# Performance work log

Hardware: AMD Instinct MI355X
Metric: run time of the kernel (lower is better)

## Reference

```python
import jax, jax.numpy as jnp
import numpy as np

HID = 3072; HEADS = 24; HD = HID // HEADS; MLP = 4 * HID; RANK = 32
B = 1; L = 2048


def setup_inputs():
    key = jax.random.key(0)
    ks = jax.random.split(key, 16)
    def rn(i, shape, s):
        return jax.random.normal(ks[i], shape, dtype=jnp.float32) * s
    x = jax.random.normal(ks[0], (B, L, HID), dtype=jnp.float32)
    vec = jax.random.normal(ks[1], (B, HID), dtype=jnp.float32)
    # Flux-style rope rotation matrices: pe shape (1, 1, L, HD//2, 2, 2)
    pos = jnp.arange(L, dtype=jnp.float32)
    inv_freq = 1.0 / (10000.0 ** (jnp.arange(HD // 2, dtype=jnp.float32) / (HD // 2)))
    ang = pos[:, None] * inv_freq[None, :]
    cos, sin = jnp.cos(ang), jnp.sin(ang)
    pe = jnp.stack([jnp.stack([cos, -sin], -1), jnp.stack([sin, cos], -1)], -2)[None, None]
    return {
        "x": x, "vec": vec, "pe": pe,
        "mod_w": rn(2, (3 * HID, HID), 0.02), "mod_b": jnp.zeros((3 * HID,), jnp.float32),
        "w1": rn(3, (3 * HID + MLP, HID), 0.02), "b1": jnp.zeros((3 * HID + MLP,), jnp.float32),
        "w2": rn(4, (HID, HID + MLP), 0.02), "b2": jnp.zeros((HID,), jnp.float32),
        "q_scale": jnp.ones((HD,), jnp.float32), "k_scale": jnp.ones((HD,), jnp.float32),
        "lora_q_down": rn(5, (RANK, HID), 1.0 / RANK), "lora_q_up": rn(6, (HID, RANK), 0.02),
        "lora_k_down": rn(7, (RANK, HID), 1.0 / RANK), "lora_k_up": rn(8, (HID, RANK), 0.02),
        "lora_v_down": rn(9, (RANK, HID), 1.0 / RANK), "lora_v_up": rn(10, (HID, RANK), 0.02),
        "proj_down": rn(11, (2 * RANK, HID + MLP), 1.0 / (2 * RANK)),
        "proj_up": rn(12, (HID, 2 * RANK), 0.02),
    }


def _rms(t, scale, eps=1e-6):
    # QKNorm: per-head-dim RMSNorm with learnable scale
    return t * jax.lax.rsqrt(jnp.mean(t * t, axis=-1, keepdims=True) + eps) * scale


def _rope(t, pe):
    # t: (B, H, L, D); pe: (1, 1, L, D//2, 2, 2)
    tr = t.reshape(*t.shape[:-1], -1, 1, 2)
    out = pe[..., 0] * tr[..., 0] + pe[..., 1] * tr[..., 1]
    return out.reshape(t.shape)


def reference(x, vec, pe, mod_w, mod_b, w1, b1, w2, b2, q_scale, k_scale,
              lora_q_down, lora_q_up, lora_k_down, lora_k_up,
              lora_v_down, lora_v_up, proj_down, proj_up):
    lora_w = 1.0  # lora_weight; note network_alpha/rank == 1 for the defaults
    # Modulation: Linear(SiLU(vec)) -> shift, scale, gate, each (B, 1, HID)
    m = jax.nn.silu(vec) @ mod_w.T + mod_b
    shift, scale, gate = [s[:, None, :] for s in jnp.split(m, 3, axis=-1)]
    # pre_norm: LayerNorm without affine, eps=1e-6
    mu = jnp.mean(x, axis=-1, keepdims=True)
    var = jnp.mean((x - mu) ** 2, axis=-1, keepdims=True)
    x_mod = (1.0 + scale) * ((x - mu) * jax.lax.rsqrt(var + 1e-6)) + shift
    # linear1 -> qkv | mlp split
    h = x_mod @ w1.T + b1                                        # (B, L, 3*HID+MLP)
    qkv, mlp = h[..., :3 * HID], h[..., 3 * HID:]
    qkv = qkv.reshape(B, L, 3, HEADS, HD).transpose(2, 0, 3, 1, 4)  # (3, B, H, L, D)
    q, k, v = qkv[0], qkv[1], qkv[2]
    def lora(down, up):
        y = ((x_mod @ down.T) @ up.T) * lora_w                   # (B, L, HID)
        return y.reshape(B, L, HEADS, HD).transpose(0, 2, 1, 3)  # (B, H, L, D)
    q = q + lora(lora_q_down, lora_q_up)
    k = k + lora(lora_k_down, lora_k_up)
    v = v + lora(lora_v_down, lora_v_up)
    q = _rms(q, q_scale)
    k = _rms(k, k_scale)
    # Bank write (self.bank_img_{q,k,v} = q, k, v) is state capture, not math.
    q = _rope(q, pe)
    k = _rope(k, pe)
    # SDPA
    scores = jnp.einsum('bhqd,bhkd->bhqk', q, k) / jnp.sqrt(jnp.float32(HD))
    attn = jax.nn.softmax(scores, axis=-1)
    attn_out = jnp.einsum('bhqk,bhkd->bhqd', attn, v)
    attn_out = attn_out.transpose(0, 2, 1, 3).reshape(B, L, HID)  # B L (H D)
    cat = jnp.concatenate([attn_out, jax.nn.gelu(mlp, approximate=True)], axis=-1)
    out = cat @ w2.T + b2
    out = out + ((cat @ proj_down.T) @ proj_up.T) * lora_w
    return x + gate * out
```

## Files before the change

kernel.cpp:

```cpp
#include <hip/hip_runtime.h>
#include <math.h>

typedef unsigned short u16;
typedef unsigned int u32;
typedef unsigned long long u64;
typedef __attribute__((ext_vector_type(4))) float f32x4;
typedef __attribute__((ext_vector_type(8))) __bf16 bf16x8;

#define SEQ 2048
#define N1 21504
#define K1 3072
#define CATK 15360

__device__ __forceinline__ u16 f2bf(float f){
  u32 u = __float_as_uint(f);
  u32 r = u + 0x7FFFu + ((u >> 16) & 1u);
  return (u16)(r >> 16);
}
__device__ __forceinline__ float bf2f(u16 h){
  return __uint_as_float(((u32)h) << 16);
}
__device__ __forceinline__ void gl_lds16(const void* g, void* l){
  __builtin_amdgcn_global_load_lds(
      (const __attribute__((address_space(1))) void*)(size_t)g,
      (__attribute__((address_space(3))) void*)(u32)(size_t)l, 16, 0, 0);
}
__device__ __forceinline__ f32x4 zero4(){ f32x4 z; z[0]=0.f; z[1]=0.f; z[2]=0.f; z[3]=0.f; return z; }

__global__ void __launch_bounds__(256) cast_w1_tail(
    const float* __restrict__ w1, u16* __restrict__ out)
{
  int gid = blockIdx.x*256 + threadIdx.x;
  int n = 9216 + gid / 384;
  int k8 = (gid - (n-9216)*384) * 8;
  const float* src = &w1[(size_t)n*K1 + k8];
  union { u16 u[8]; uint4 q; } t;
  #pragma unroll
  for (int j=0;j<8;j++) t.u[j] = f2bf(src[j]);
  *(uint4*)&out[(size_t)n*K1 + k8] = t.q;
}

__global__ void __launch_bounds__(256) build_ustack(
    const float* __restrict__ lqu, const float* __restrict__ lku,
    const float* __restrict__ lvu, u16* __restrict__ out)
{
  int gid = blockIdx.x*256 + threadIdx.x;
  int n = gid >> 4;
  int k8 = (gid & 15) * 8;
  int b = n / 3072;
  const float* up = (b==0)? lqu : (b==1)? lku : lvu;
  int nl = n - b*3072;
  union { u16 u[8]; uint4 q; } t;
  #pragma unroll
  for (int j=0;j<8;j++){
    int r = k8 + j - 32*b;
    t.u[j] = (r >= 0 && r < 32) ? f2bf(up[(size_t)nl*32 + r]) : (u16)0;
  }
  *(uint4*)&out[(size_t)n*128 + k8] = t.q;
}

__global__ void __launch_bounds__(256) build_dcatT(
    const float* __restrict__ lqd, const float* __restrict__ lkd,
    const float* __restrict__ lvd, u16* __restrict__ out)
{
  int gid = blockIdx.x*256 + threadIdx.x;
  int k = gid >> 4;
  int r8 = (gid & 15) * 8;
  union { u16 u[8]; uint4 q; } t;
  #pragma unroll
  for (int j=0;j<8;j++){
    int r = r8 + j;
    float v = (r < 32) ? lqd[(size_t)r*3072 + k]
            : (r < 64) ? lkd[(size_t)(r-32)*3072 + k]
            : (r < 96) ? lvd[(size_t)(r-64)*3072 + k] : 0.f;
    t.u[j] = f2bf(v);
  }
  *(uint4*)&out[(size_t)k*128 + r8] = t.q;
}

__global__ void __launch_bounds__(256) build_pubf(
    const float* __restrict__ pu, u16* __restrict__ out)
{
  int gid = blockIdx.x*256 + threadIdx.x;
  int n = gid >> 3;
  int r8 = (gid & 7) * 8;
  union { u16 u[8]; uint4 q; } t;
  #pragma unroll
  for (int j=0;j<8;j++) t.u[j] = f2bf(pu[(size_t)n*64 + r8 + j]);
  *(uint4*)&out[(size_t)n*64 + r8] = t.q;
}

__global__ void __launch_bounds__(256) build_pdT(
    const float* __restrict__ pd, u16* __restrict__ out)
{
  int gid = blockIdx.x*256 + threadIdx.x;
  int jj = gid >> 3;
  int r8 = (gid & 7) * 8;
  union { u16 u[8]; uint4 q; } t;
  #pragma unroll
  for (int j=0;j<8;j++) t.u[j] = f2bf(pd[(size_t)(r8+j)*15360 + jj]);
  *(uint4*)&out[(size_t)jj*64 + r8] = t.q;
}

__global__ void __launch_bounds__(256) silu_kernel(const float* __restrict__ v, float* __restrict__ sv){
  int i = blockIdx.x*256 + threadIdx.x;
  float x = v[i];
  sv[i] = x / (1.f + __expf(-x));
}

__global__ void __launch_bounds__(256) modgemv_kernel(
    const float* __restrict__ sv, const float* __restrict__ mw,
    const float* __restrict__ mb, float* __restrict__ mout)
{
  int n = blockIdx.x, tid = threadIdx.x;
  const float* wr = mw + (size_t)n*3072;
  float p = 0.f;
  for (int c = tid; c < 3072; c += 256) p += sv[c]*wr[c];
  #pragma unroll
  for (int o=32;o>0;o>>=1) p += __shfl_down(p,o,64);
  __shared__ float red[4];
  if ((tid & 63)==0) red[tid>>6] = p;
  __syncthreads();
  if (tid==0) mout[n] = red[0]+red[1]+red[2]+red[3] + mb[n];
}

__global__ void __launch_bounds__(256) xmod_kernel(
    const float* __restrict__ x, const float* __restrict__ m, u16* __restrict__ xm)
{
  int l = blockIdx.x, tid = threadIdx.x;
  const float* xr = x + (size_t)l*3072;
  float s1=0.f, s2=0.f;
  for (int c=tid;c<3072;c+=256){ float v = xr[c]; s1+=v; s2+=v*v; }
  #pragma unroll
  for (int o=32;o>0;o>>=1){ s1 += __shfl_down(s1,o,64); s2 += __shfl_down(s2,o,64); }
  __shared__ float r1[4], r2[4];
  if ((tid&63)==0){ r1[tid>>6]=s1; r2[tid>>6]=s2; }
  __syncthreads();
  float su = r1[0]+r1[1]+r1[2]+r1[3];
  float sq = r2[0]+r2[1]+r2[2]+r2[3];
  float mu = su / 3072.f;
  float var = sq/3072.f - mu*mu;
  float rstd = rsqrtf(var + 1e-6f);
  u16* orow = xm + (size_t)l*K1;
  for (int c=tid;c<3072;c+=256){
    float v = (xr[c]-mu)*rstd;
    v = v*(1.f + m[3072+c]) + m[c];
    orow[c] = f2bf(v);
  }
}

__global__ void __launch_bounds__(256) gelu_kernel(const u16* __restrict__ h, u16* __restrict__ cat){
  int j = blockIdx.x*256 + threadIdx.x;
  int l = blockIdx.y;
  float v = bf2f(h[(size_t)l*N1 + 9216 + j]);
  float u = 0.7978845608028654f * (v + 0.044715f*v*v*v);
  float t = 1.f - 2.f/(__expf(2.f*u) + 1.f);
  cat[(size_t)l*CATK + 3072 + j] = f2bf(0.5f*v*(1.f + t));
}

__global__ void __launch_bounds__(128) qkv_kernel(
    const u16* __restrict__ h, const float* __restrict__ pe,
    const float* __restrict__ qs, const float* __restrict__ ks,
    u16* __restrict__ qbf, u16* __restrict__ kbf)
{
  const int l = blockIdx.x, hh = blockIdx.y, d = threadIdx.x;
  __shared__ float lq[128], lk[128];
  __shared__ float red[4];
  size_t base = (size_t)l*N1 + (size_t)hh*128 + d;
  float qv = bf2f(h[base]);
  float kv = bf2f(h[base + 3072]);
  float pq = qv*qv, pk = kv*kv;
  #pragma unroll
  for (int o=32;o>0;o>>=1){ pq += __shfl_down(pq,o,64); pk += __shfl_down(pk,o,64); }
  if ((d & 63)==0){ red[(d>>6)*2] = pq; red[(d>>6)*2+1] = pk; }
  __syncthreads();
  float rq = rsqrtf((red[0]+red[2])/128.f + 1e-6f);
  float rk = rsqrtf((red[1]+red[3])/128.f + 1e-6f);
  lq[d] = qv*rq*qs[d];
  lk[d] = kv*rk*ks[d];
  __syncthreads();
  int i = d >> 1;
  const float* peb = pe + ((size_t)l*64 + i)*4 + (size_t)(d&1)*2;
  float qo = peb[0]*lq[2*i] + peb[1]*lq[2*i+1];
  float ko = peb[0]*lk[2*i] + peb[1]*lk[2*i+1];
  size_t ob = ((size_t)hh*SEQ + l)*128 + d;
  qbf[ob] = f2bf(qo);
  kbf[ob] = f2bf(ko);
}

template<int MODE>
__global__ void __launch_bounds__(256) gemm_bt(
    const u16* __restrict__ A, const u16* __restrict__ B, void* __restrict__ C,
    int K, int lda, int ldb, int ldc, int ldadd,
    const float* __restrict__ bias, const float* __restrict__ xres,
    const float* __restrict__ gate)
{
  __shared__ u16 sA[128*64];
  __shared__ u16 sB[128*64];
  const int tid = threadIdx.x;
  const int lane = tid & 63;
  const int wv = tid >> 6;
  const int quad = lane >> 4;
  const int l16 = lane & 15;
  const int rw = (wv >> 1) * 64;
  const int cw = (wv & 1) * 64;
  const int m0 = blockIdx.x * 128;
  const int n0 = blockIdx.y * 128;

  f32x4 acc[4][4];
  #pragma unroll
  for (int i=0;i<4;i++){
    #pragma unroll
    for (int j=0;j<4;j++) acc[i][j] = zero4();
  }

  for (int kb = 0; kb < K; kb += 64){
    #pragma unroll
    for (int i=0;i<4;i++){
      int c = i*256 + tid, r = c >> 3, s = c & 7, g = s ^ (r & 7);
      gl_lds16(A + (size_t)(m0 + r)*lda + kb + g*8, &sA[c*8]);
    }
    #pragma unroll
    for (int i=0;i<4;i++){
      int c = i*256 + tid, r = c >> 3, s = c & 7, g = s ^ (r & 7);
      gl_lds16(B + (size_t)(n0 + r)*ldb + kb + g*8, &sB[c*8]);
    }
    __syncthreads();
    #pragma unroll
    for (int kc=0; kc<2; kc++){
      bf16x8 af[4], bfr[4];
      #pragma unroll
      for (int mt=0; mt<4; mt++){
        int row = rw + mt*16 + l16;
        int s = (kc*4 + quad) ^ (row & 7);
        af[mt] = *(const bf16x8*)&sA[row*64 + s*8];
      }
      #pragma unroll
      for (int nt=0; nt<4; nt++){
        int row = cw + nt*16 + l16;
        int s = (kc*4 + quad) ^ (row & 7);
        bfr[nt] = *(const bf16x8*)&sB[row*64 + s*8];
      }
      #pragma unroll
      for (int mt=0; mt<4; mt++){
        #pragma unroll
        for (int nt=0; nt<4; nt++)
          acc[mt][nt] = __builtin_amdgcn_mfma_f32_16x16x32_bf16(af[mt], bfr[nt], acc[mt][nt], 0, 0, 0);
      }
    }
    __syncthreads();
  }

  #pragma unroll
  for (int mt=0; mt<4; mt++){
    #pragma unroll
    for (int nt=0; nt<4; nt++){
      #pragma unroll
      for (int r=0;r<4;r++){
        int row = m0 + rw + mt*16 + quad*4 + r;
        int col = n0 + cw + nt*16 + l16;
        float v = acc[mt][nt][r];
        if (MODE==0){
          v += bias[col];
          ((u16*)C)[(size_t)row*ldc + col] = f2bf(v);
        } else if (MODE==1){
          v += bias[col];
          ((float*)C)[(size_t)row*ldc + col] = xres[(size_t)row*3072 + col] + gate[col]*v;
        } else {
          v += xres[(size_t)row*ldadd + col];
          ((u16*)C)[(size_t)row*ldc + col] = f2bf(v);
        }
      }
    }
  }
}


#define CFENCE asm volatile("" ::: "memory")
#define VMCNT(n) asm volatile("s_waitcnt vmcnt(" #n ")" ::: "memory")

__device__ __forceinline__ void stA64(const u16* __restrict__ g, u16* __restrict__ lds,
                                      int rb, int kb, int lda, int tid){
  int ri = tid >> 3, s = tid & 7;
  int R = rb + ri;
  gl_lds16(g + (size_t)R*lda + kb + ((s ^ (R & 7)) << 3), &lds[(R << 6) + (s << 3)]);
}
__device__ __forceinline__ void stB32x2(const u16* __restrict__ g, u16* __restrict__ lds,
                                        int rb, int kb, int ldb, int tid){
  int ri = tid >> 3, s = tid & 7;
  int R = rb + (ri & 31) + ((ri >> 5) << 6);
  gl_lds16(g + (size_t)R*ldb + kb + ((s ^ (R & 7)) << 3), &lds[(R << 6) + (s << 3)]);
}

__global__ void __launch_bounds__(512, 2) gemm256_bias(
    const u16* __restrict__ A, const u16* __restrict__ B, u16* __restrict__ C,
    int K, int lda, int ldb, int ldc, const float* __restrict__ bias)
{
  __shared__ u16 sA[2][256*64];
  __shared__ u16 sB[2][256*64];
  const int tid  = threadIdx.x;
  const int lane = tid & 63;
  const int wv   = tid >> 6;
  const int quad = lane >> 4;
  const int l16  = lane & 15;
  const int wm   = wv >> 2;
  const int wn   = wv & 3;
  const int m0   = blockIdx.x * 256;
  const int n0   = blockIdx.y * 256;
  const u16* Ab  = A + (size_t)m0 * lda;
  const u16* Bb  = B + (size_t)n0 * ldb;
  const int NT   = K >> 6;

  f32x4 acc[8][4];
  #pragma unroll
  for (int i=0;i<8;i++){
    #pragma unroll
    for (int j=0;j<4;j++) acc[i][j] = zero4();
  }

  stA64 (Ab, sA[0],   0, 0, lda, tid);  stA64 (Ab, sA[0], 128, 0, lda, tid);
  stB32x2(Bb, sB[0],  0, 0, ldb, tid);  stB32x2(Bb, sB[0], 128, 0, ldb, tid);
  stA64 (Ab, sA[0],  64, 0, lda, tid);  stA64 (Ab, sA[0], 192, 0, lda, tid);
  stB32x2(Bb, sB[0], 32, 0, ldb, tid);  stB32x2(Bb, sB[0], 160, 0, ldb, tid);
  if (NT > 1){
    stA64 (Ab, sA[1],   0, 64, lda, tid);  stA64 (Ab, sA[1], 128, 64, lda, tid);
    stB32x2(Bb, sB[1],  0, 64, ldb, tid);  stB32x2(Bb, sB[1], 128, 64, ldb, tid);
  }
  VMCNT(4);
  CFENCE; __builtin_amdgcn_s_barrier(); CFENCE;

  bf16x8 af[4][2], bf0[2][2], bf1[2][2];

#define LDA_Q(QM) \
  _Pragma("unroll") \
  for (int mt=0; mt<4; ++mt){ \
    int row = wm*128 + ((QM)*4+mt)*16 + l16; \
    _Pragma("unroll") \
    for (int kc=0; kc<2; ++kc){ \
      int s = (kc*4+quad) ^ (row & 7); \
      af[mt][kc] = *(const bf16x8*)&sAb[row*64 + s*8]; \
    } \
  }

#define LDB_Q(dst, QN) \
  _Pragma("unroll") \
  for (int nt=0; nt<2; ++nt){ \
    int row = wn*64 + ((QN)*2+nt)*16 + l16; \
    _Pragma("unroll") \
    for (int kc=0; kc<2; ++kc){ \
      int s = (kc*4+quad) ^ (row & 7); \
      dst[nt][kc] = *(const bf16x8*)&sBb[row*64 + s*8]; \
    } \
  }

#define PHASE_MFMA(bfX, QM, QN) \
  __builtin_amdgcn_s_setprio(1); \
  _Pragma("unroll") \
  for (int mt=0; mt<4; ++mt){ \
    _Pragma("unroll") \
    for (int kc=0; kc<2; ++kc){ \
      _Pragma("unroll") \
      for (int nt=0; nt<2; ++nt) \
        acc[(QM)*4+mt][(QN)*2+nt] = __builtin_amdgcn_mfma_f32_16x16x32_bf16( \
            af[mt][kc], bfX[nt][kc], acc[(QM)*4+mt][(QN)*2+nt], 0, 0, 0); \
    } \
  } \
  __builtin_amdgcn_s_setprio(0);

  for (int t = 0; t < NT; ++t){
    const int buf = t & 1;
    const u16* sAb = sA[buf];
    const u16* sBb = sB[buf];
    u16* sAc = sA[buf];
    u16* sBc = sB[buf];
    u16* sAn = sA[buf ^ 1];
    u16* sBn = sB[buf ^ 1];
    const int kb1 = (t+1) << 6;
    const int kb2 = (t+2) << 6;
    const bool p1 = (t+1 < NT);
    const bool p2 = (t+2 < NT);

    LDA_Q(0)
    LDB_Q(bf0, 0)
    if (p1){ stA64(Ab, sAn, 64, kb1, lda, tid); stA64(Ab, sAn, 192, kb1, lda, tid); }
    CFENCE; __builtin_amdgcn_s_barrier(); CFENCE;
    PHASE_MFMA(bf0, 0, 0)
    if (p1){ VMCNT(6); } else { VMCNT(0); }
    CFENCE; __builtin_amdgcn_s_barrier(); CFENCE;

    LDB_Q(bf1, 1)
    if (p1){ stB32x2(Bb, sBn, 32, kb1, ldb, tid); stB32x2(Bb, sBn, 160, kb1, ldb, tid); }
    CFENCE; __builtin_amdgcn_s_barrier(); CFENCE;
    PHASE_MFMA(bf1, 0, 1)
    CFENCE; __builtin_amdgcn_s_barrier(); CFENCE;

    LDA_Q(1)
    if (p2){ stA64(Ab, sAc, 0, kb2, lda, tid); stA64(Ab, sAc, 128, kb2, lda, tid); }
    CFENCE; __builtin_amdgcn_s_barrier(); CFENCE;
    PHASE_MFMA(bf0, 1, 0)
    CFENCE; __builtin_amdgcn_s_barrier(); CFENCE;

    if (p2){ stB32x2(Bb, sBc, 0, kb2, ldb, tid); stB32x2(Bb, sBc, 128, kb2, ldb, tid); }
    CFENCE; __builtin_amdgcn_s_barrier(); CFENCE;
    PHASE_MFMA(bf1, 1, 1)
    if (p2){ VMCNT(8); } else if (p1){ VMCNT(4); } else { VMCNT(0); }
    CFENCE; __builtin_amdgcn_s_barrier(); CFENCE;
  }

#undef LDA_Q
#undef LDB_Q
#undef PHASE_MFMA

  #pragma unroll
  for (int mt=0; mt<8; ++mt){
    #pragma unroll
    for (int nt=0; nt<4; ++nt){
      #pragma unroll
      for (int r=0;r<4;++r){
        int row = m0 + wm*128 + mt*16 + quad*4 + r;
        int col = n0 + wn*64 + nt*16 + l16;
        float v = acc[mt][nt][r] + bias[col];
        C[(size_t)row*ldc + col] = f2bf(v);
      }
    }
  }
}

__global__ void __launch_bounds__(256) attn_kernel(
    const u16* __restrict__ qbf, const u16* __restrict__ kbf,
    const u16* __restrict__ h, u16* __restrict__ cat)
{
  __shared__ u16 sQ[64*128];
  __shared__ u16 sK[64*128];
  __shared__ u16 sVT[128*64];
  __shared__ u16 sP[4*16*64];

  const int tid = threadIdx.x;
  const int lane = tid & 63;
  const int wv = tid >> 6;
  const int quad = lane >> 4;
  const int l16 = lane & 15;
  const int l0 = blockIdx.x * 64;
  const int hh = blockIdx.y;

  const u16* qb = qbf + (size_t)hh*SEQ*128;
  const u16* kbp = kbf + (size_t)hh*SEQ*128;

  #pragma unroll
  for (int i=0;i<4;i++){
    int c = i*256 + tid, r = c >> 4, s = c & 15, g = s ^ (r & 15);
    gl_lds16(qb + (size_t)(l0 + r)*128 + g*8, &sQ[c*8]);
  }

  const int kv8 = tid >> 5;
  const int d4  = (tid & 31) * 4;

  f32x4 accO[8];
  #pragma unroll
  for (int i=0;i<8;i++) accO[i] = zero4();
  float m_i[4] = {-INFINITY,-INFINITY,-INFINITY,-INFINITY};
  float l_i[4] = {0.f,0.f,0.f,0.f};

  for (int kv0 = 0; kv0 < SEQ; kv0 += 64){
    #pragma unroll
    for (int i=0;i<4;i++){
      int c = i*256 + tid, r = c >> 4, s = c & 15, g = s ^ (r & 15);
      gl_lds16(kbp + (size_t)(kv0 + r)*128 + g*8, &sK[c*8]);
    }
    {
      const u16* src = h + (size_t)(kv0 + kv8*8)*N1 + 6144 + (size_t)hh*128 + d4;
      u64 vv[8];
      #pragma unroll
      for (int j=0;j<8;j++) vv[j] = *(const u64*)(src + (size_t)j*N1);
      #pragma unroll
      for (int jd=0;jd<4;jd++){
        int d = d4 + jd;
        union { u16 u[8]; uint4 q; } t;
        #pragma unroll
        for (int j=0;j<8;j++) t.u[j] = (u16)(vv[j] >> (16*jd));
        int s = kv8 ^ (d & 7) ^ ((d >> 3) & 7);
        *(uint4*)&sVT[d*64 + s*8] = t.q;
      }
    }
    __syncthreads();

    f32x4 sacc[4];
    #pragma unroll
    for (int i=0;i<4;i++) sacc[i] = zero4();
    __builtin_amdgcn_s_setprio(1);
    #pragma unroll
    for (int kc=0; kc<4; kc++){
      int arow = wv*16 + l16;
      int as = (kc*4 + quad) ^ (arow & 15);
      bf16x8 aF = *(const bf16x8*)&sQ[arow*128 + as*8];
      #pragma unroll
      for (int nt=0; nt<4; nt++){
        int brow = nt*16 + l16;
        int bs = (kc*4 + quad) ^ (brow & 15);
        bf16x8 bF = *(const bf16x8*)&sK[brow*128 + bs*8];
        sacc[nt] = __builtin_amdgcn_mfma_f32_16x16x32_bf16(aF, bF, sacc[nt], 0, 0, 0);
      }
    }
    __builtin_amdgcn_s_setprio(0);
    const float scl = 0.08838834764831845f;
    #pragma unroll
    for (int nt=0; nt<4; nt++){
      #pragma unroll
      for (int r=0;r<4;r++) sacc[nt][r] *= scl;
    }

    float alpha[4];
    #pragma unroll
    for (int r=0;r<4;r++){
      float v = fmaxf(fmaxf(sacc[0][r],sacc[1][r]), fmaxf(sacc[2][r],sacc[3][r]));
      v = fmaxf(v, __shfl_xor(v,1,64));
      v = fmaxf(v, __shfl_xor(v,2,64));
      v = fmaxf(v, __shfl_xor(v,4,64));
      v = fmaxf(v, __shfl_xor(v,8,64));
      float mnew = fmaxf(m_i[r], v);
      alpha[r] = __expf(m_i[r] - mnew);
      m_i[r] = mnew;
    }
    float p[4][4];
    float rsum[4] = {0.f,0.f,0.f,0.f};
    #pragma unroll
    for (int nt=0; nt<4; nt++){
      #pragma unroll
      for (int r=0;r<4;r++){
        float pv = __expf(sacc[nt][r] - m_i[r]);
        p[nt][r] = pv;
        rsum[r] += pv;
      }
    }
    #pragma unroll
    for (int r=0;r<4;r++){
      float s = rsum[r];
      s += __shfl_xor(s,1,64); s += __shfl_xor(s,2,64);
      s += __shfl_xor(s,4,64); s += __shfl_xor(s,8,64);
      l_i[r] = l_i[r]*alpha[r] + s;
    }
    u16* pw = &sP[wv*1024];
    #pragma unroll
    for (int nt=0; nt<4; nt++){
      #pragma unroll
      for (int r=0;r<4;r++){
        int rloc = quad*4 + r;
        int c = nt*16 + l16;
        int slot = (c >> 3) ^ (rloc & 7);
        pw[rloc*64 + slot*8 + (c & 7)] = f2bf(p[nt][r]);
      }
    }
    #pragma unroll
    for (int dt=0; dt<8; dt++){
      #pragma unroll
      for (int r=0;r<4;r++) accO[dt][r] *= alpha[r];
    }
    int prow = l16;
    int ps0 = quad ^ (prow & 7);
    int ps1 = (4 + quad) ^ (prow & 7);
    bf16x8 p0 = *(const bf16x8*)&pw[prow*64 + ps0*8];
    bf16x8 p1 = *(const bf16x8*)&pw[prow*64 + ps1*8];
    __builtin_amdgcn_s_setprio(1);
    #pragma unroll
    for (int dt=0; dt<8; dt++){
      int vrow = dt*16 + l16;
      int hs = (vrow >> 3) & 7;
      int vs0 = (quad ^ (vrow & 7) ^ hs);
      int vs1 = ((4 + quad) ^ (vrow & 7) ^ hs);
      bf16x8 v0 = *(const bf16x8*)&sVT[vrow*64 + vs0*8];
      bf16x8 v1 = *(const bf16x8*)&sVT[vrow*64 + vs1*8];
      accO[dt] = __builtin_amdgcn_mfma_f32_16x16x32_bf16(p0, v0, accO[dt], 0, 0, 0);
      accO[dt] = __builtin_amdgcn_mfma_f32_16x16x32_bf16(p1, v1, accO[dt], 0, 0, 0);
    }
    __builtin_amdgcn_s_setprio(0);
    __syncthreads();
  }

  #pragma unroll
  for (int dt=0; dt<8; dt++){
    #pragma unroll
    for (int r=0;r<4;r++){
      int row = l0 + wv*16 + quad*4 + r;
      int col = hh*128 + dt*16 + l16;
      cat[(size_t)row*CATK + col] = f2bf(accO[dt][r] / l_i[r]);
    }
  }
}

extern "C" void kernel_launch(void* const* d_in, const int* in_sizes, int n_in,
                              void* d_out, int out_size, void* d_ws, size_t ws_size,
                              hipStream_t stream)
{
  (void)in_sizes; (void)n_in; (void)out_size; (void)ws_size;
  const float* x    = (const float*)d_in[0];
  const float* vec  = (const float*)d_in[1];
  const float* pe   = (const float*)d_in[2];
  const float* modw = (const float*)d_in[3];
  const float* modb = (const float*)d_in[4];
  const float* w1   = (const float*)d_in[5];
  const float* b1   = (const float*)d_in[6];
  const float* w2   = (const float*)d_in[7];
  const float* b2   = (const float*)d_in[8];
  const float* qs   = (const float*)d_in[9];
  const float* ks   = (const float*)d_in[10];
  const float* lqd  = (const float*)d_in[11];
  const float* lqu  = (const float*)d_in[12];
  const float* lkd  = (const float*)d_in[13];
  const float* lku  = (const float*)d_in[14];
  const float* lvd  = (const float*)d_in[15];
  const float* lvu  = (const float*)d_in[16];
  const float* pd   = (const float*)d_in[17];
  const float* pu   = (const float*)d_in[18];
  float* out = (float*)d_out;

  char* ws = (char*)d_ws;
  float* sv    = (float*)(ws + 0);
  float* mvec  = (float*)(ws + 12288);
  u16* xm      = (u16*)(ws + 49152);
  u16* U       = (u16*)(ws + 12632064);
  u16* DT      = (u16*)(ws + 14991360);
  u16* pubf    = (u16*)(ws + 15777792);
  u16* pdT     = (u16*)(ws + 16171008);
  u16* w1ext   = (u16*)(ws + 18137088);
  u16* w2ext   = (u16*)(ws + 150257664);
  u16* hbuf    = (u16*)(ws + 244629504);
  u16* qbf     = (u16*)(ws + 332709888);
  u16* kbf     = (u16*)(ws + 345292800);
  u16* cat     = (u16*)(ws + 357875712);

  cast_w1_tail<<<18432,256,0,stream>>>(w1, w1ext);
  build_ustack<<<576,256,0,stream>>>(lqu,lku,lvu,U);
  build_dcatT<<<192,256,0,stream>>>(lqd,lkd,lvd,DT);
  build_pubf<<<96,256,0,stream>>>(pu,pubf);
  build_pdT<<<480,256,0,stream>>>(pd,pdT);
  gemm_bt<3><<<dim3(72,24),256,0,stream>>>(U,DT,(void*)w1ext,
      128,128,128,K1,K1,nullptr,w1,nullptr);
  gemm_bt<3><<<dim3(24,120),256,0,stream>>>(pubf,pdT,(void*)w2ext,
      64,64,64,CATK,CATK,nullptr,w2,nullptr);

  silu_kernel<<<12,256,0,stream>>>(vec,sv);
  modgemv_kernel<<<9216,256,0,stream>>>(sv,modw,modb,mvec);
  xmod_kernel<<<2048,256,0,stream>>>(x,mvec,xm);
  gemm256_bias<<<dim3(8,84),512,0,stream>>>(xm,w1ext,hbuf,K1,K1,K1,N1,b1);
  qkv_kernel<<<dim3(2048,24),128,0,stream>>>(hbuf,pe,qs,ks,qbf,kbf);
  gelu_kernel<<<dim3(48,2048),256,0,stream>>>(hbuf,cat);
  attn_kernel<<<dim3(32,24),256,0,stream>>>(qbf,kbf,hbuf,cat);
  gemm_bt<1><<<dim3(16,24),256,0,stream>>>(cat,w2ext,(void*)out,
      CATK,CATK,CATK,3072,0,b2,x,mvec+6144);
}
```

Measured before the change: 1.511 ms.

## Run the output projection GEMM as a split-K 256x256 pipelined kernel with atomics

The final cat@w2 GEMM (K=15360) moves from the simple 128x128 single-buffered gemm_bt to the double-buffered 256x256 MFMA pipeline, shared through a macro body. K is split 8 ways so the grid has 768 blocks, and each block accumulates into an fp32 scratch buffer with atomic adds. A zeroing kernel and a separate vectorized epilogue apply the bias, gate and residual. This trades better tile reuse and occupancy for extra atomic traffic, two extra launches, and a scratch buffer that reuses the already-consumed xm/U/w1ext region.

```diff
diff --git a/kernel.cpp b/kernel.cpp
--- a/kernel.cpp
+++ b/kernel.cpp
@@ -188,6 +188,29 @@
   kbf[ob] = f2bf(ko);
 }
 
+__global__ void __launch_bounds__(256) zero_f32(float* __restrict__ p){
+  ((f32x4*)p)[blockIdx.x*256 + threadIdx.x] = zero4();
+}
+
+__global__ void __launch_bounds__(256) final_epilogue(
+    const float* __restrict__ S, const float* __restrict__ x,
+    const float* __restrict__ gate, const float* __restrict__ b2,
+    float* __restrict__ out)
+{
+  int row = blockIdx.x;
+  int c4  = blockIdx.y*256 + threadIdx.x;
+  size_t i = (size_t)row*768 + c4;
+  int col4 = c4 * 4;
+  f32x4 s = ((const f32x4*)S)[i];
+  f32x4 xv = ((const f32x4*)x)[i];
+  f32x4 g = *(const f32x4*)&gate[col4];
+  f32x4 b = *(const f32x4*)&b2[col4];
+  f32x4 o;
+  #pragma unroll
+  for (int j=0;j<4;j++) o[j] = xv[j] + g[j]*(s[j] + b[j]);
+  ((f32x4*)out)[i] = o;
+}
+
 template<int MODE>
 __global__ void __launch_bounds__(256) gemm_bt(
     const u16* __restrict__ A, const u16* __restrict__ B, void* __restrict__ C,
@@ -263,9 +286,6 @@
         if (MODE==0){
           v += bias[col];
           ((u16*)C)[(size_t)row*ldc + col] = f2bf(v);
-        } else if (MODE==1){
-          v += bias[col];
-          ((float*)C)[(size_t)row*ldc + col] = xres[(size_t)row*3072 + col] + gate[col]*v;
         } else {
           v += xres[(size_t)row*ldadd + col];
           ((u16*)C)[(size_t)row*ldc + col] = f2bf(v);
@@ -291,6 +311,96 @@
   int R = rb + (ri & 31) + ((ri >> 5) << 6);
   gl_lds16(g + (size_t)R*ldb + kb + ((s ^ (R & 7)) << 3), &lds[(R << 6) + (s << 3)]);
 }
+
+#define LDA_Q(QM) \
+  _Pragma("unroll") \
+  for (int mt=0; mt<4; ++mt){ \
+    int row = wm*128 + ((QM)*4+mt)*16 + l16; \
+    _Pragma("unroll") \
+    for (int kc=0; kc<2; ++kc){ \
+      int s = (kc*4+quad) ^ (row & 7); \
+      af[mt][kc] = *(const bf16x8*)&sAb[row*64 + s*8]; \
+    } \
+  }
+
+#define LDB_Q(dst, QN) \
+  _Pragma("unroll") \
+  for (int nt=0; nt<2; ++nt){ \
+    int row = wn*64 + ((QN)*2+nt)*16 + l16; \
+    _Pragma("unroll") \
+    for (int kc=0; kc<2; ++kc){ \
+      int s = (kc*4+quad) ^ (row & 7); \
+      dst[nt][kc] = *(const bf16x8*)&sBb[row*64 + s*8]; \
+    } \
+  }
+
+#define PHASE_MFMA(bfX, QM, QN) \
+  __builtin_amdgcn_s_setprio(1); \
+  _Pragma("unroll") \
+  for (int mt=0; mt<4; ++mt){ \
+    _Pragma("unroll") \
+    for (int kc=0; kc<2; ++kc){ \
+      _Pragma("unroll") \
+      for (int nt=0; nt<2; ++nt) \
+        acc[(QM)*4+mt][(QN)*2+nt] = __builtin_amdgcn_mfma_f32_16x16x32_bf16( \
+            af[mt][kc], bfX[nt][kc], acc[(QM)*4+mt][(QN)*2+nt], 0, 0, 0); \
+    } \
+  } \
+  __builtin_amdgcn_s_setprio(0);
+
+#define GEMM256_BODY \
+  f32x4 acc[8][4]; \
+  _Pragma("unroll") \
+  for (int i=0;i<8;i++){ \
+    _Pragma("unroll") \
+    for (int j=0;j<4;j++) acc[i][j] = zero4(); \
+  } \
+  stA64 (Ab, sA[0],   0, 0, lda, tid);  stA64 (Ab, sA[0], 128, 0, lda, tid); \
+  stB32x2(Bb, sB[0],  0, 0, ldb, tid);  stB32x2(Bb, sB[0], 128, 0, ldb, tid); \
+  stA64 (Ab, sA[0],  64, 0, lda, tid);  stA64 (Ab, sA[0], 192, 0, lda, tid); \
+  stB32x2(Bb, sB[0], 32, 0, ldb, tid);  stB32x2(Bb, sB[0], 160, 0, ldb, tid); \
+  if (NT > 1){ \
+    stA64 (Ab, sA[1],   0, 64, lda, tid);  stA64 (Ab, sA[1], 128, 64, lda, tid); \
+    stB32x2(Bb, sB[1],  0, 64, ldb, tid);  stB32x2(Bb, sB[1], 128, 64, ldb, tid); \
+  } \
+  VMCNT(4); \
+  CFENCE; __builtin_amdgcn_s_barrier(); CFENCE; \
+  bf16x8 af[4][2], bf0[2][2], bf1[2][2]; \
+  for (int t = 0; t < NT; ++t){ \
+    const int buf = t & 1; \
+    const u16* sAb = sA[buf]; \
+    const u16* sBb = sB[buf]; \
+    u16* sAc = sA[buf]; \
+    u16* sBc = sB[buf]; \
+    u16* sAn = sA[buf ^ 1]; \
+    u16* sBn = sB[buf ^ 1]; \
+    const int kb1 = (t+1) << 6; \
+    const int kb2 = (t+2) << 6; \
+    const bool p1 = (t+1 < NT); \
+    const bool p2 = (t+2 < NT); \
+    LDA_Q(0) \
+    LDB_Q(bf0, 0) \
+    if (p1){ stA64(Ab, sAn, 64, kb1, lda, tid); stA64(Ab, sAn, 192, kb1, lda, tid); } \
+    CFENCE; __builtin_amdgcn_s_barrier(); CFENCE; \
+    PHASE_MFMA(bf0, 0, 0) \
+    if (p1){ VMCNT(6); } else { VMCNT(0); } \
+    CFENCE; __builtin_amdgcn_s_barrier(); CFENCE; \
+    LDB_Q(bf1, 1) \
+    if (p1){ stB32x2(Bb, sBn, 32, kb1, ldb, tid); stB32x2(Bb, sBn, 160, kb1, ldb, tid); } \
+    CFENCE; __builtin_amdgcn_s_barrier(); CFENCE; \
+    PHASE_MFMA(bf1, 0, 1) \
+    CFENCE; __builtin_amdgcn_s_barrier(); CFENCE; \
+    LDA_Q(1) \
+    if (p2){ stA64(Ab, sAc, 0, kb2, lda, tid); stA64(Ab, sAc, 128, kb2, lda, tid); } \
+    CFENCE; __builtin_amdgcn_s_barrier(); CFENCE; \
+    PHASE_MFMA(bf0, 1, 0) \
+    CFENCE; __builtin_amdgcn_s_barrier(); CFENCE; \
+    if (p2){ stB32x2(Bb, sBc, 0, kb2, ldb, tid); stB32x2(Bb, sBc, 128, kb2, ldb, tid); } \
+    CFENCE; __builtin_amdgcn_s_barrier(); CFENCE; \
+    PHASE_MFMA(bf1, 1, 1) \
+    if (p2){ VMCNT(8); } else if (p1){ VMCNT(4); } else { VMCNT(0); } \
+    CFENCE; __builtin_amdgcn_s_barrier(); CFENCE; \
+  }
 
 __global__ void __launch_bounds__(512, 2) gemm256_bias(
     const u16* __restrict__ A, const u16* __restrict__ B, u16* __restrict__ C,
@@ -311,105 +421,7 @@
   const u16* Bb  = B + (size_t)n0 * ldb;
   const int NT   = K >> 6;
 
-  f32x4 acc[8][4];
-  #pragma unroll
-  for (int i=0;i<8;i++){
-    #pragma unroll
-    for (int j=0;j<4;j++) acc[i][j] = zero4();
-  }
-
-  stA64 (Ab, sA[0],   0, 0, lda, tid);  stA64 (Ab, sA[0], 128, 0, lda, tid);
-  stB32x2(Bb, sB[0],  0, 0, ldb, tid);  stB32x2(Bb, sB[0], 128, 0, ldb, tid);
-  stA64 (Ab, sA[0],  64, 0, lda, tid);  stA64 (Ab, sA[0], 192, 0, lda, tid);
-  stB32x2(Bb, sB[0], 32, 0, ldb, tid);  stB32x2(Bb, sB[0], 160, 0, ldb, tid);
-  if (NT > 1){
-    stA64 (Ab, sA[1],   0, 64, lda, tid);  stA64 (Ab, sA[1], 128, 64, lda, tid);
-    stB32x2(Bb, sB[1],  0, 64, ldb, tid);  stB32x2(Bb, sB[1], 128, 64, ldb, tid);
-  }
-  VMCNT(4);
-  CFENCE; __builtin_amdgcn_s_barrier(); CFENCE;
-
-  bf16x8 af[4][2], bf0[2][2], bf1[2][2];
-
-#define LDA_Q(QM) \
-  _Pragma("unroll") \
-  for (int mt=0; mt<4; ++mt){ \
-    int row = wm*128 + ((QM)*4+mt)*16 + l16; \
-    _Pragma("unroll") \
-    for (int kc=0; kc<2; ++kc){ \
-      int s = (kc*4+quad) ^ (row & 7); \
-      af[mt][kc] = *(const bf16x8*)&sAb[row*64 + s*8]; \
-    } \
-  }
-
-#define LDB_Q(dst, QN) \
-  _Pragma("unroll") \
-  for (int nt=0; nt<2; ++nt){ \
-    int row = wn*64 + ((QN)*2+nt)*16 + l16; \
-    _Pragma("unroll") \
-    for (int kc=0; kc<2; ++kc){ \
-      int s = (kc*4+quad) ^ (row & 7); \
-      dst[nt][kc] = *(const bf16x8*)&sBb[row*64 + s*8]; \
-    } \
-  }
-
-#define PHASE_MFMA(bfX, QM, QN) \
-  __builtin_amdgcn_s_setprio(1); \
-  _Pragma("unroll") \
-  for (int mt=0; mt<4; ++mt){ \
-    _Pragma("unroll") \
-    for (int kc=0; kc<2; ++kc){ \
-      _Pragma("unroll") \
-      for (int nt=0; nt<2; ++nt) \
-        acc[(QM)*4+mt][(QN)*2+nt] = __builtin_amdgcn_mfma_f32_16x16x32_bf16( \
-            af[mt][kc], bfX[nt][kc], acc[(QM)*4+mt][(QN)*2+nt], 0, 0, 0); \
-    } \
-  } \
-  __builtin_amdgcn_s_setprio(0);
-
-  for (int t = 0; t < NT; ++t){
-    const int buf = t & 1;
-    const u16* sAb = sA[buf];
-    const u16* sBb = sB[buf];
-    u16* sAc = sA[buf];
-    u16* sBc = sB[buf];
-    u16* sAn = sA[buf ^ 1];
-    u16* sBn = sB[buf ^ 1];
-    const int kb1 = (t+1) << 6;
-    const int kb2 = (t+2) << 6;
-    const bool p1 = (t+1 < NT);
-    const bool p2 = (t+2 < NT);
-
-    LDA_Q(0)
-    LDB_Q(bf0, 0)
-    if (p1){ stA64(Ab, sAn, 64, kb1, lda, tid); stA64(Ab, sAn, 192, kb1, lda, tid); }
-    CFENCE; __builtin_amdgcn_s_barrier(); CFENCE;
-    PHASE_MFMA(bf0, 0, 0)
-    if (p1){ VMCNT(6); } else { VMCNT(0); }
-    CFENCE; __builtin_amdgcn_s_barrier(); CFENCE;
-
-    LDB_Q(bf1, 1)
-    if (p1){ stB32x2(Bb, sBn, 32, kb1, ldb, tid); stB32x2(Bb, sBn, 160, kb1, ldb, tid); }
-    CFENCE; __builtin_amdgcn_s_barrier(); CFENCE;
-    PHASE_MFMA(bf1, 0, 1)
-    CFENCE; __builtin_amdgcn_s_barrier(); CFENCE;
-
-    LDA_Q(1)
-    if (p2){ stA64(Ab, sAc, 0, kb2, lda, tid); stA64(Ab, sAc, 128, kb2, lda, tid); }
-    CFENCE; __builtin_amdgcn_s_barrier(); CFENCE;
-    PHASE_MFMA(bf0, 1, 0)
-    CFENCE; __builtin_amdgcn_s_barrier(); CFENCE;
-
-    if (p2){ stB32x2(Bb, sBc, 0, kb2, ldb, tid); stB32x2(Bb, sBc, 128, kb2, ldb, tid); }
-    CFENCE; __builtin_amdgcn_s_barrier(); CFENCE;
-    PHASE_MFMA(bf1, 1, 1)
-    if (p2){ VMCNT(8); } else if (p1){ VMCNT(4); } else { VMCNT(0); }
-    CFENCE; __builtin_amdgcn_s_barrier(); CFENCE;
-  }
-
-#undef LDA_Q
-#undef LDB_Q
-#undef PHASE_MFMA
+  GEMM256_BODY
 
   #pragma unroll
   for (int mt=0; mt<8; ++mt){
@@ -425,6 +437,47 @@
     }
   }
 }
+
+__global__ void __launch_bounds__(512, 2) gemm256_splitk(
+    const u16* __restrict__ A, const u16* __restrict__ B, float* __restrict__ S,
+    int KS, int lda, int ldb, int ldc)
+{
+  __shared__ u16 sA[2][256*64];
+  __shared__ u16 sB[2][256*64];
+  const int tid  = threadIdx.x;
+  const int lane = tid & 63;
+  const int wv   = tid >> 6;
+  const int quad = lane >> 4;
+  const int l16  = lane & 15;
+  const int wm   = wv >> 2;
+  const int wn   = wv & 3;
+  const int m0   = blockIdx.x * 256;
+  const int n0   = blockIdx.y * 256;
+  const int kbase = blockIdx.z * KS;
+  const u16* Ab  = A + (size_t)m0 * lda + kbase;
+  const u16* Bb  = B + (size_t)n0 * ldb + kbase;
+  const int NT   = KS >> 6;
+
+  GEMM256_BODY
+
+  #pragma unroll
+  for (int mt=0; mt<8; ++mt){
+    #pragma unroll
+    for (int nt=0; nt<4; ++nt){
+      #pragma unroll
+      for (int r=0;r<4;++r){
+        int row = m0 + wm*128 + mt*16 + quad*4 + r;
+        int col = n0 + wn*64 + nt*16 + l16;
+        unsafeAtomicAdd(&S[(size_t)row*ldc + col], acc[mt][nt][r]);
+      }
+    }
+  }
+}
+
+#undef LDA_Q
+#undef LDB_Q
+#undef PHASE_MFMA
+#undef GEMM256_BODY
 
 __global__ void __launch_bounds__(256) attn_kernel(
     const u16* __restrict__ qbf, const u16* __restrict__ kbf,
@@ -617,6 +670,7 @@
   float* sv    = (float*)(ws + 0);
   float* mvec  = (float*)(ws + 12288);
   u16* xm      = (u16*)(ws + 49152);
+  float* Sacc  = (float*)(ws + 49152);
   u16* U       = (u16*)(ws + 12632064);
   u16* DT      = (u16*)(ws + 14991360);
   u16* pubf    = (u16*)(ws + 15777792);
@@ -642,9 +696,11 @@
   modgemv_kernel<<<9216,256,0,stream>>>(sv,modw,modb,mvec);
   xmod_kernel<<<2048,256,0,stream>>>(x,mvec,xm);
   gemm256_bias<<<dim3(8,84),512,0,stream>>>(xm,w1ext,hbuf,K1,K1,K1,N1,b1);
+  zero_f32<<<6144,256,0,stream>>>(Sacc);
   qkv_kernel<<<dim3(2048,24),128,0,stream>>>(hbuf,pe,qs,ks,qbf,kbf);
   gelu_kernel<<<dim3(48,2048),256,0,stream>>>(hbuf,cat);
   attn_kernel<<<dim3(32,24),256,0,stream>>>(qbf,kbf,hbuf,cat);
-  gemm_bt<1><<<dim3(16,24),256,0,stream>>>(cat,w2ext,(void*)out,
-      CATK,CATK,CATK,3072,0,b2,x,mvec+6144);
-}
+  gemm256_splitk<<<dim3(8,12,8),512,0,stream>>>(cat,w2ext,Sacc,
+      CATK/8,CATK,CATK,3072);
+  final_epilogue<<<dim3(2048,3),256,0,stream>>>(Sacc,x,mvec+6144,b2,out);
+}
```

New measurement: 1.497 ms. About the same (-0.9%).
